# Kernel tuning notes

Hardware: AMD Instinct MI355X
Metric: run time of the kernel (lower is better)

## Reference

```python
import jax, jax.numpy as jnp
import numpy as np

LATENT = 40

def setup_inputs() -> dict:
    key = jax.random.key(0)
    k1, k2, k3, k4 = jax.random.split(key, 4)
    B, P, O = 32768, 2048, 200
    return {
        "input": jax.random.normal(k1, (B, LATENT), dtype=jnp.float32),
        "prototypes": jax.random.uniform(k2, (P, LATENT), dtype=jnp.float32),
        "w": jax.random.normal(k3, (O, P), dtype=jnp.float32) * 0.02,
        "b": jax.random.normal(k4, (O,), dtype=jnp.float32) * 0.02,
    }

def reference(input, prototypes, w, b):
    # Faithful to the original: each row of x is a SINGLE scalar
    # sqrt(sum over ALL prototypes and latent dims of (x_i - P)^2),
    # broadcast across the n_prototypes columns.
    x = input.astype(jnp.float32).reshape(input.shape[0], LATENT)  # (B, 40)
    P = prototypes.shape[0]
    proto_sum = jnp.sum(prototypes, axis=0)            # (40,)
    proto_sq = jnp.sum(prototypes * prototypes)        # scalar
    s = (P * jnp.sum(x * x, axis=1)                    # (B,)
         - 2.0 * (x @ proto_sum)
         + proto_sq)
    d = jnp.sqrt(s)                                    # (B,)
    xmat = jnp.broadcast_to(d[:, None], (x.shape[0], P))  # (B, P)
    out = xmat @ w.T + b                               # (B, O)
    min1 = jnp.mean(jnp.min(xmat, axis=0))             # scalar
    min2 = jnp.mean(jnp.min(xmat, axis=1))             # scalar
    return (min1, min2, out)
```

## Files before the change

### kernel.cpp

```cpp
#include <hip/hip_runtime.h>

#define NPROTO 2048
#define NOUT   200
#define LAT    40
#define PBLK   16
#define FBLK   1024
#define RPB    32
#define NB1    64


__global__ __launch_bounds__(320) void pc_stage1(const float* __restrict__ protos,
                                                 const float* __restrict__ w,
                                                 float* __restrict__ ws) {
    const int b = blockIdx.x;
    const int t = threadIdx.x;
    __shared__ float sred[5];
    __shared__ float sdim[8][40];
    __shared__ float ssq[5];
    if (b == 0) {
        if (t < NB1) ((int*)ws)[6400 + t * 32] = 0;
        if (t == NB1) ((int*)ws)[8448] = 0;
    }
    if (b < NOUT) {
        float acc = 0.f;
        const float4* row = (const float4*)(w + b * NPROTO);
        float4 v0 = row[t];
        acc += v0.x + v0.y + v0.z + v0.w;
        if (t < 192) {
            float4 v1 = row[t + 320];
            acc += v1.x + v1.y + v1.z + v1.w;
        }
        #pragma unroll
        for (int off = 32; off > 0; off >>= 1) acc += __shfl_down(acc, off, 64);
        if ((t & 63) == 0) sred[t >> 6] = acc;
        __syncthreads();
        if (t == 0) ws[b] = sred[0] + sred[1] + sred[2] + sred[3] + sred[4];
    } else {
        const int rel = b - NOUT;
        const int d = t % 40, g = t / 40;
        float sum = 0.f, sq = 0.f;
        for (int idx = rel * 320 + t; idx < NPROTO * LAT; idx += PBLK * 320) {
            float v = protos[idx];
            sum += v;
            sq  += v * v;
        }
        sdim[g][d] = sum;
        #pragma unroll
        for (int off = 32; off > 0; off >>= 1) sq += __shfl_down(sq, off, 64);
        if ((t & 63) == 0) ssq[t >> 6] = sq;
        __syncthreads();
        if (t < 40) {
            float s = 0.f;
            #pragma unroll
            for (int g2 = 0; g2 < 8; ++g2) s += sdim[g2][t];
            ws[256 + rel * 40 + t] = s;
        }
        if (t == 0) ws[200 + rel] = ssq[0] + ssq[1] + ssq[2] + ssq[3] + ssq[4];
    }
}

__device__ __forceinline__ unsigned long long pack2f(float a, float b) {
    union { float f[2]; unsigned long long u; } c;
    c.f[0] = a; c.f[1] = b; return c.u;
}

__global__ __launch_bounds__(256) void pc_distout(const float* __restrict__ x,
                                                  const float* __restrict__ bias,
                                                  float* __restrict__ ws,
                                                  float* __restrict__ out) {
    __shared__ float4 sx[RPB * 10];
    __shared__ float  sps[40];
    __shared__ float  spsq;
    __shared__ float2 swb[100];
    __shared__ float2 sbb[100];
    __shared__ float  sd[RPB];
    __shared__ int    islast;
    __shared__ float  fmn[4], fsm[4];
    const int t   = threadIdx.x;
    const int blk = blockIdx.x;

    {
        const float4* xs = (const float4*)(x + blk * (RPB * LAT));
        sx[t] = xs[t];
        if (t < RPB * 10 - 256) sx[t + 256] = xs[t + 256];
    }

    if (t < 40) {
        float s = 0.f;
        #pragma unroll
        for (int j = 0; j < PBLK; ++j) s += ws[256 + j * 40 + t];
        sps[t] = s;
    } else if (t == 40) {
        float s = 0.f;
        #pragma unroll
        for (int j = 0; j < PBLK; ++j) s += ws[200 + j];
        spsq = s;
    }
    if (t >= 56 && t < 156) swb[t - 56]  = ((const float2*)ws)[t - 56];
    if (t >= 156)           sbb[t - 156] = ((const float2*)bias)[t - 156];
    __syncthreads();

    float pmn = 0.f, psm = 0.f;
    if (t < RPB) {
        float ssq2 = 0.f, dot = 0.f;
        #pragma unroll
        for (int k = 0; k < 10; ++k) {
            float4 v = sx[t * 10 + k];
            ssq2 += v.x * v.x + v.y * v.y + v.z * v.z + v.w * v.w;
            dot  += v.x * sps[4 * k] + v.y * sps[4 * k + 1] +
                    v.z * sps[4 * k + 2] + v.w * sps[4 * k + 3];
        }
        const float d = sqrtf(2048.f * ssq2 - 2.f * dot + spsq);
        sd[t] = d;
        float mn = d, sm = d;
        #pragma unroll
        for (int off = 16; off > 0; off >>= 1) {
            mn = fminf(mn, __shfl_down(mn, off, 64));
            sm += __shfl_down(sm, off, 64);
        }
        pmn = mn; psm = sm;
    }
    __syncthreads();

    float2* o = (float2*)(out + 2);
    const int base = blk * (RPB * 100);
    for (int idx = t; idx < RPB * 100; idx += 256) {
        const int i = idx / 100;
        const int j = idx - i * 100;
        const float  dd = sd[i];
        const float2 wv = swb[j];
        const float2 bv = sbb[j];
        float2 r;
        r.x = dd * wv.x + bv.x;
        r.y = dd * wv.y + bv.y;
        o[base + idx] = r;
    }

    unsigned long long* pptr = (unsigned long long*)ws + 1024;
    int* cnt1 = (int*)ws + 6400;
    int* cnt2 = (int*)ws + 8448;
    if (t == 0) {
        __hip_atomic_store(pptr + blk, pack2f(pmn, psm),
                           __ATOMIC_RELAXED, __HIP_MEMORY_SCOPE_AGENT);
        asm volatile("s_waitcnt vmcnt(0)" ::: "memory");
        const int c = blk & (NB1 - 1);
        int last = 0;
        int p1 = __hip_atomic_fetch_add(cnt1 + c * 32, 1, __ATOMIC_RELAXED,
                                        __HIP_MEMORY_SCOPE_AGENT);
        if (p1 == FBLK / NB1 - 1) {
            int p2 = __hip_atomic_fetch_add(cnt2, 1, __ATOMIC_RELAXED,
                                            __HIP_MEMORY_SCOPE_AGENT);
            last = (p2 == NB1 - 1);
        }
        islast = last;
    }
    __syncthreads();

    if (islast) {
        float mn = 3.4e38f, sm = 0.f;
        #pragma unroll
        for (int j = 0; j < FBLK / 256; ++j) {
            unsigned long long v = __hip_atomic_load(pptr + j * 256 + t,
                                                     __ATOMIC_RELAXED,
                                                     __HIP_MEMORY_SCOPE_AGENT);
            union { unsigned long long u; float f[2]; } c2; c2.u = v;
            mn = fminf(mn, c2.f[0]);
            sm += c2.f[1];
        }
        #pragma unroll
        for (int off = 32; off > 0; off >>= 1) {
            mn = fminf(mn, __shfl_down(mn, off, 64));
            sm += __shfl_down(sm, off, 64);
        }
        if ((t & 63) == 0) { fmn[t >> 6] = mn; fsm[t >> 6] = sm; }
        __syncthreads();
        if (t == 0) {
            out[0] = fminf(fminf(fmn[0], fmn[1]), fminf(fmn[2], fmn[3]));
            out[1] = (fsm[0] + fsm[1] + fsm[2] + fsm[3]) * (1.0f / 32768.0f);
        }
    }
}

extern "C" void kernel_launch(void* const* d_in, const int* in_sizes, int n_in,
                              void* d_out, int out_size, void* d_ws, size_t ws_size,
                              hipStream_t stream) {
    const float* x      = (const float*)d_in[0];
    const float* protos = (const float*)d_in[1];
    const float* w      = (const float*)d_in[2];
    const float* bias   = (const float*)d_in[3];
    float* out = (float*)d_out;
    float* ws  = (float*)d_ws;

    pc_stage1<<<NOUT + PBLK, 320, 0, stream>>>(protos, w, ws);
    pc_distout<<<FBLK, 256, 0, stream>>>(x, bias, ws, out);
}
```

Before: 18.85 us.

## Vectorize output stores to aligned float4 and halve rows per block

```diff
diff --git a/kernel.cpp b/kernel.cpp
--- a/kernel.cpp
+++ b/kernel.cpp
@@ -4,8 +4,8 @@
 #define NOUT   200
 #define LAT    40
 #define PBLK   16
-#define FBLK   1024
-#define RPB    32
+#define FBLK   2048
+#define RPB    16
 #define NB1    64
 
 
@@ -68,21 +68,22 @@
                                                   const float* __restrict__ bias,
                                                   float* __restrict__ ws,
                                                   float* __restrict__ out) {
-    __shared__ float4 sx[RPB * 10];
     __shared__ float  sps[40];
     __shared__ float  spsq;
-    __shared__ float2 swb[100];
-    __shared__ float2 sbb[100];
+    __shared__ float4 swb4[49];
+    __shared__ float4 sbb4[49];
+    __shared__ float2 shw, stw, shb, stb;
     __shared__ float  sd[RPB];
     __shared__ int    islast;
     __shared__ float  fmn[4], fsm[4];
     const int t   = threadIdx.x;
     const int blk = blockIdx.x;
 
-    {
-        const float4* xs = (const float4*)(x + blk * (RPB * LAT));
-        sx[t] = xs[t];
-        if (t < RPB * 10 - 256) sx[t + 256] = xs[t + 256];
+    float4 xv[10];
+    if (t < RPB) {
+        const float4* xr = (const float4*)(x + (blk * RPB + t) * LAT);
+        #pragma unroll
+        for (int k = 0; k < 10; ++k) xv[k] = xr[k];
     }
 
     if (t < 40) {
@@ -95,9 +96,22 @@
         #pragma unroll
         for (int j = 0; j < PBLK; ++j) s += ws[200 + j];
         spsq = s;
-    }
-    if (t >= 56 && t < 156) swb[t - 56]  = ((const float2*)ws)[t - 56];
-    if (t >= 156)           sbb[t - 156] = ((const float2*)bias)[t - 156];
+    } else if (t >= 41 && t < 90) {
+        const int j = t - 41;
+        const float2* w2 = (const float2*)ws;
+        float2 a = w2[1 + 2 * j], b = w2[2 + 2 * j];
+        swb4[j] = make_float4(a.x, a.y, b.x, b.y);
+    } else if (t >= 90 && t < 139) {
+        const int j = t - 90;
+        const float2* b2 = (const float2*)bias;
+        float2 a = b2[1 + 2 * j], b = b2[2 + 2 * j];
+        sbb4[j] = make_float4(a.x, a.y, b.x, b.y);
+    } else if (t == 139) {
+        shw = make_float2(ws[0], ws[1]);
+        stw = make_float2(ws[198], ws[199]);
+        shb = make_float2(bias[0], bias[1]);
+        stb = make_float2(bias[198], bias[199]);
+    }
     __syncthreads();
 
     float pmn = 0.f, psm = 0.f;
@@ -105,7 +119,7 @@
         float ssq2 = 0.f, dot = 0.f;
         #pragma unroll
         for (int k = 0; k < 10; ++k) {
-            float4 v = sx[t * 10 + k];
+            float4 v = xv[k];
             ssq2 += v.x * v.x + v.y * v.y + v.z * v.z + v.w * v.w;
             dot  += v.x * sps[4 * k] + v.y * sps[4 * k + 1] +
                     v.z * sps[4 * k + 2] + v.w * sps[4 * k + 3];
@@ -114,7 +128,7 @@
         sd[t] = d;
         float mn = d, sm = d;
         #pragma unroll
-        for (int off = 16; off > 0; off >>= 1) {
+        for (int off = 8; off > 0; off >>= 1) {
             mn = fminf(mn, __shfl_down(mn, off, 64));
             sm += __shfl_down(sm, off, 64);
         }
@@ -122,18 +136,30 @@
     }
     __syncthreads();
 
-    float2* o = (float2*)(out + 2);
-    const int base = blk * (RPB * 100);
-    for (int idx = t; idx < RPB * 100; idx += 256) {
-        const int i = idx / 100;
-        const int j = idx - i * 100;
+    float* const obase = out + 2 + blk * (RPB * NOUT);
+    for (int idx = t; idx < RPB * 49; idx += 256) {
+        const int i = idx / 49;
+        const int j = idx - i * 49;
         const float  dd = sd[i];
-        const float2 wv = swb[j];
-        const float2 bv = sbb[j];
-        float2 r;
+        const float4 wv = swb4[j];
+        const float4 bv = sbb4[j];
+        float4 r;
         r.x = dd * wv.x + bv.x;
         r.y = dd * wv.y + bv.y;
-        o[base + idx] = r;
+        r.z = dd * wv.z + bv.z;
+        r.w = dd * wv.w + bv.w;
+        *(float4*)(obase + i * NOUT + 2 + 4 * j) = r;
+    }
+    if (t < 2 * RPB) {
+        const int r = t >> 1;
+        const float dd = sd[r];
+        if (t & 1) {
+            float2 v; v.x = dd * stw.x + stb.x; v.y = dd * stw.y + stb.y;
+            *(float2*)(obase + r * NOUT + 198) = v;
+        } else {
+            float2 v; v.x = dd * shw.x + shb.x; v.y = dd * shw.y + shb.y;
+            *(float2*)(obase + r * NOUT) = v;
+        }
     }
 
     unsigned long long* pptr = (unsigned long long*)ws + 1024;
```

Measured after the change: 20.28 us. 1.08x slower.
